# Kernel optimization log

Measured on AMD Instinct MI355X. Metric: run time of the kernel, lower is better.

## Reference

```python
import jax, jax.numpy as jnp
import numpy as np

# BlendParams defaults (pytorch3d)
SIGMA = 1e-4
GAMMA = 1e-4
ZNEAR = 1.0
ZFAR = 100.0
EPS = 1e-10

N, H, W, K, C = 4, 256, 256, 8, 16
V, F = 100000, 200000


def setup_inputs() -> dict:
    key = jax.random.key(0)
    ks = jax.random.split(key, 7)
    return {
        "dists": jax.random.normal(ks[0], (N, H, W, K), dtype=jnp.float32),
        "zbuf": jax.random.uniform(ks[1], (N, H, W, K), dtype=jnp.float32),
        "bary_coords": jax.random.uniform(ks[2], (N, H, W, K, 3), dtype=jnp.float32),
        "verts_features": jax.random.normal(ks[3], (V, C), dtype=jnp.float32),
        "background": jax.random.uniform(ks[4], (C,), dtype=jnp.float32),
        "pix_to_face": jax.random.randint(ks[5], (N, H, W, K), 0, F),
        "faces": jax.random.randint(ks[6], (F, 3), 0, V),
    }


def reference(dists, zbuf, bary_coords, verts_features, background, pix_to_face, faces):
    mask = (pix_to_face >= 0)
    maskf = mask.astype(dists.dtype)
    safe_idx = jnp.where(mask, pix_to_face, 0)

    # --- sample_textures (TexturesVertex): barycentric gather ---
    # faces[safe_idx]: (N,H,W,K,3) vertex ids -> (N,H,W,K,3,C) features
    face_vert_feats = verts_features[faces[safe_idx]]
    texels = jnp.einsum("nhwkv,nhwkvc->nhwkc", bary_coords, face_vert_feats)

    # --- softmax_blend ---
    prob_map = jax.nn.sigmoid(-dists / SIGMA) * maskf                 # (N,H,W,K)
    z_inv = (ZFAR - zbuf) / (ZFAR - ZNEAR) * maskf                    # (N,H,W,K)
    z_inv_max = jnp.clip(jnp.max(z_inv, axis=-1, keepdims=True), EPS)  # (N,H,W,1)
    weights_num = prob_map * jnp.exp((z_inv - z_inv_max) / GAMMA)      # (N,H,W,K)
    delta = jnp.clip(jnp.exp((EPS - z_inv_max) / GAMMA), EPS)          # (N,H,W,1)
    denom = jnp.sum(weights_num, axis=-1, keepdims=True) + delta       # (N,H,W,1)

    weighted_colors = jnp.einsum("nhwk,nhwkc->nhwc", weights_num, texels)
    pixel_colors = (weighted_colors + delta * background) / denom      # (N,H,W,C)
    return pixel_colors
```

## Files before the change

kernel.cpp:

```cpp
#include <hip/hip_runtime.h>


constexpr int KK = 8;
constexpr int CC = 16;

__global__ __launch_bounds__(256) void feature_shader(
    const float* __restrict__ dists,
    const float* __restrict__ zbuf,
    const float* __restrict__ bary,
    const float* __restrict__ vfeat,
    const float* __restrict__ bg,
    const int*   __restrict__ p2f,
    const int*   __restrict__ faces,
    float* __restrict__ out,
    int n)
{
    const float INV_SIGMA = 1e4f;
    const float INV_GAMMA = 1e4f;
    const float EPS       = 1e-10f;
    const float ZFAR      = 100.f;
    const float INV_SPAN  = 1.f / 99.f;

    int t = blockIdx.x * blockDim.x + threadIdx.x;
    if (t >= n) return;
    int k = t & (KK - 1);

    float z  = zbuf[t];
    float dd = dists[t];
    int   f  = p2f[t];

    float zinv = (f >= 0) ? (ZFAR - z) * INV_SPAN : 0.f;

    float m = zinv;
    m = fmaxf(m, __shfl_xor(m, 1));
    m = fmaxf(m, __shfl_xor(m, 2));
    m = fmaxf(m, __shfl_xor(m, 4));
    m = fmaxf(m, EPS);

    float delta = fmaxf(__expf((EPS - m) * INV_GAMMA), EPS);
    float prob  = (f >= 0) ? 1.f / (1.f + __expf(dd * INV_SIGMA)) : 0.f;
    float w     = prob * __expf((zinv - m) * INV_GAMMA);

    float denom = w;
    denom += __shfl_xor(denom, 1);
    denom += __shfl_xor(denom, 2);
    denom += __shfl_xor(denom, 4);
    denom += delta;
    float thr = denom * 1e-7f;

    float acc[CC];
    #pragma unroll
    for (int c = 0; c < CC; ++c) acc[c] = 0.f;

    if (w > thr) {
        int v0 = faces[f * 3 + 0];
        int v1 = faces[f * 3 + 1];
        int v2 = faces[f * 3 + 2];
        const float* bp = bary + (size_t)t * 3;
        float b0 = bp[0] * w, b1 = bp[1] * w, b2 = bp[2] * w;
        const float4* t0 = (const float4*)(vfeat + (size_t)v0 * CC);
        const float4* t1 = (const float4*)(vfeat + (size_t)v1 * CC);
        const float4* t2 = (const float4*)(vfeat + (size_t)v2 * CC);
        #pragma unroll
        for (int j = 0; j < 4; ++j) {
            float4 a0 = t0[j], a1 = t1[j], a2 = t2[j];
            acc[j * 4 + 0] = b0 * a0.x + b1 * a1.x + b2 * a2.x;
            acc[j * 4 + 1] = b0 * a0.y + b1 * a1.y + b2 * a2.y;
            acc[j * 4 + 2] = b0 * a0.z + b1 * a1.z + b2 * a2.z;
            acc[j * 4 + 3] = b0 * a0.w + b1 * a1.w + b2 * a2.w;
        }
    }

    {
        bool low = (k & 4) == 0;
        float nxt[8];
        #pragma unroll
        for (int i = 0; i < 8; ++i) {
            float send = low ? acc[8 + i] : acc[i];
            float recv = __shfl_xor(send, 4);
            nxt[i] = (low ? acc[i] : acc[8 + i]) + recv;
        }
        #pragma unroll
        for (int i = 0; i < 8; ++i) acc[i] = nxt[i];
    }
    {
        bool low = (k & 2) == 0;
        float nxt[4];
        #pragma unroll
        for (int i = 0; i < 4; ++i) {
            float send = low ? acc[4 + i] : acc[i];
            float recv = __shfl_xor(send, 2);
            nxt[i] = (low ? acc[i] : acc[4 + i]) + recv;
        }
        #pragma unroll
        for (int i = 0; i < 4; ++i) acc[i] = nxt[i];
    }
    {
        bool low = (k & 1) == 0;
        float nxt[2];
        #pragma unroll
        for (int i = 0; i < 2; ++i) {
            float send = low ? acc[2 + i] : acc[i];
            float recv = __shfl_xor(send, 1);
            nxt[i] = (low ? acc[i] : acc[2 + i]) + recv;
        }
        acc[0] = nxt[0];
        acc[1] = nxt[1];
    }

    float2 g = ((const float2*)bg)[k];
    float inv_den = 1.f / denom;
    float2 o;
    o.x = (acc[0] + delta * g.x) * inv_den;
    o.y = (acc[1] + delta * g.y) * inv_den;
    ((float2*)out)[t] = o;
}

extern "C" void kernel_launch(void* const* d_in, const int* in_sizes, int n_in,
                              void* d_out, int out_size, void* d_ws, size_t ws_size,
                              hipStream_t stream) {
    const float* dists = (const float*)d_in[0];
    const float* zbuf  = (const float*)d_in[1];
    const float* bary  = (const float*)d_in[2];
    const float* vfeat = (const float*)d_in[3];
    const float* bg    = (const float*)d_in[4];
    const int*   p2f   = (const int*)d_in[5];
    const int*   faces = (const int*)d_in[6];
    float* out = (float*)d_out;

    int n = in_sizes[0];
    int block = 256;
    int grid = (n + block - 1) / block;

    hipLaunchKernelGGL(feature_shader, dim3(grid), dim3(block), 0, stream,
                       dists, zbuf, bary, vfeat, bg, p2f, faces, out, n);
}
```

Baseline: 120.5 us.

## Cooperatively gather texel features per pixel group instead of per-layer full gather

```diff
diff --git a/kernel.cpp b/kernel.cpp
--- a/kernel.cpp
+++ b/kernel.cpp
@@ -2,9 +2,8 @@
 
 
 constexpr int KK = 8;
-constexpr int CC = 16;
 
-__global__ __launch_bounds__(256) void feature_shader(
+__global__ __launch_bounds__(256) void feature_shader_r3(
     const float* __restrict__ dists,
     const float* __restrict__ zbuf,
     const float* __restrict__ bary,
@@ -23,7 +22,10 @@
 
     int t = blockIdx.x * blockDim.x + threadIdx.x;
     if (t >= n) return;
-    int k = t & (KK - 1);
+    int lane = threadIdx.x & 63;
+    int c    = lane & (KK - 1);
+    int base = lane & ~(KK - 1);
+    int p    = t >> 3;
 
     float z  = zbuf[t];
     float dd = dists[t];
@@ -48,71 +50,37 @@
     denom += delta;
     float thr = denom * 1e-7f;
 
-    float acc[CC];
-    #pragma unroll
-    for (int c = 0; c < CC; ++c) acc[c] = 0.f;
+    unsigned long long bal = __ballot(w > thr);
+    unsigned gmask = (unsigned)((bal >> base) & 0xFFull);
 
-    if (w > thr) {
-        int v0 = faces[f * 3 + 0];
-        int v1 = faces[f * 3 + 1];
-        int v2 = faces[f * 3 + 2];
-        const float* bp = bary + (size_t)t * 3;
-        float b0 = bp[0] * w, b1 = bp[1] * w, b2 = bp[2] * w;
-        const float4* t0 = (const float4*)(vfeat + (size_t)v0 * CC);
-        const float4* t1 = (const float4*)(vfeat + (size_t)v1 * CC);
-        const float4* t2 = (const float4*)(vfeat + (size_t)v2 * CC);
-        #pragma unroll
-        for (int j = 0; j < 4; ++j) {
-            float4 a0 = t0[j], a1 = t1[j], a2 = t2[j];
-            acc[j * 4 + 0] = b0 * a0.x + b1 * a1.x + b2 * a2.x;
-            acc[j * 4 + 1] = b0 * a0.y + b1 * a1.y + b2 * a2.y;
-            acc[j * 4 + 2] = b0 * a0.z + b1 * a1.z + b2 * a2.z;
-            acc[j * 4 + 3] = b0 * a0.w + b1 * a1.w + b2 * a2.w;
-        }
+    float accx = 0.f, accy = 0.f;
+
+    while (gmask) {
+        int j = __builtin_ctz(gmask);
+        gmask &= gmask - 1;
+
+        float wj = __shfl(w, base | j);
+        int   fj = __shfl(f, base | j);
+
+        const float* bp = bary + (size_t)(p * KK + j) * 3;
+        float b0 = bp[0] * wj, b1 = bp[1] * wj, b2 = bp[2] * wj;
+        int v0 = faces[fj * 3 + 0];
+        int v1 = faces[fj * 3 + 1];
+        int v2 = faces[fj * 3 + 2];
+
+        float2 a0 = ((const float2*)(vfeat + (size_t)v0 * 16))[c];
+        float2 a1 = ((const float2*)(vfeat + (size_t)v1 * 16))[c];
+        float2 a2 = ((const float2*)(vfeat + (size_t)v2 * 16))[c];
+
+        accx += b0 * a0.x + b1 * a1.x + b2 * a2.x;
+        accy += b0 * a0.y + b1 * a1.y + b2 * a2.y;
     }
 
-    {
-        bool low = (k & 4) == 0;
-        float nxt[8];
-        #pragma unroll
-        for (int i = 0; i < 8; ++i) {
-            float send = low ? acc[8 + i] : acc[i];
-            float recv = __shfl_xor(send, 4);
-            nxt[i] = (low ? acc[i] : acc[8 + i]) + recv;
-        }
-        #pragma unroll
-        for (int i = 0; i < 8; ++i) acc[i] = nxt[i];
-    }
-    {
-        bool low = (k & 2) == 0;
-        float nxt[4];
-        #pragma unroll
-        for (int i = 0; i < 4; ++i) {
-            float send = low ? acc[4 + i] : acc[i];
-            float recv = __shfl_xor(send, 2);
-            nxt[i] = (low ? acc[i] : acc[4 + i]) + recv;
-        }
-        #pragma unroll
-        for (int i = 0; i < 4; ++i) acc[i] = nxt[i];
-    }
-    {
-        bool low = (k & 1) == 0;
-        float nxt[2];
-        #pragma unroll
-        for (int i = 0; i < 2; ++i) {
-            float send = low ? acc[2 + i] : acc[i];
-            float recv = __shfl_xor(send, 1);
-            nxt[i] = (low ? acc[i] : acc[2 + i]) + recv;
-        }
-        acc[0] = nxt[0];
-        acc[1] = nxt[1];
-    }
-
-    float2 g = ((const float2*)bg)[k];
+    float2 g = ((const float2*)bg)[c];
     float inv_den = 1.f / denom;
     float2 o;
-    o.x = (acc[0] + delta * g.x) * inv_den;
-    o.y = (acc[1] + delta * g.y) * inv_den;
+    o.x = (accx + delta * g.x) * inv_den;
+    o.y = (accy + delta * g.y) * inv_den;
     ((float2*)out)[t] = o;
 }
 
@@ -132,6 +100,6 @@
     int block = 256;
     int grid = (n + block - 1) / block;
 
-    hipLaunchKernelGGL(feature_shader, dim3(grid), dim3(block), 0, stream,
+    hipLaunchKernelGGL(feature_shader_r3, dim3(grid), dim3(block), 0, stream,
                        dists, zbuf, bary, vfeat, bg, p2f, faces, out, n);
 }
```

Result: slower. 123.2 us (+2.2%).
